# Performance work log

Measured on AMD Instinct MI355X. Metric: run time of the kernel, lower is better.

## Reference

```python
import jax, jax.numpy as jnp
import numpy as np
import math
from jax import lax

TAU = 2
SIGMA_D2 = (TAU / 1.5) ** 2
SIGMA_TH2 = math.radians(20.0) ** 2

_offs = range(-TAU, TAU + 1)
OFFSETS = np.array([(dz, dy, dx) for dz in _offs for dy in _offs for dx in _offs
                    if dz or dy or dx], dtype=np.int32)  # (124, 3)
W_DIST = np.exp(-(OFFSETS.astype(np.float64) ** 2).sum(1) / SIGMA_D2).astype(np.float32)


def setup_inputs() -> dict:
    key = jax.random.key(0)
    k1, k2 = jax.random.split(key)
    n_pred = jax.random.normal(k1, (2, 3, 64, 64, 64), dtype=jnp.float32)
    source_pred = jax.random.normal(k2, (2, 1, 64, 64, 64), dtype=jnp.float32)
    return {"n_pred": n_pred, "source_pred": source_pred}


def reference(n_pred, source_pred):
    B, C, D, H, W = n_pred.shape
    pad = TAU
    # F.normalize(p=2, dim=1, eps=1e-6): divide by max(norm, eps)
    norm = jnp.sqrt(jnp.sum(n_pred * n_pred, axis=1, keepdims=True))
    n = n_pred / jnp.maximum(norm, 1e-6)

    prob = jax.nn.sigmoid(source_pred)            # (B,1,D,H,W)
    central_mask = prob > 0.5                      # (B,1,D,H,W)

    spat = ((0, 0), (0, 0), (pad, pad), (pad, pad), (pad, pad))
    padded_n = jnp.pad(n, spat)                    # zero pad like F.pad value=0
    padded_p = jnp.pad(prob, spat)

    offsets = jnp.asarray(OFFSETS)                 # (124,3)
    w_dist = jnp.asarray(W_DIST, dtype=n.dtype)    # (124,)

    def body(carry, xs):
        off, wd = xs
        start_n = (0, 0, pad + off[0], pad + off[1], pad + off[2])
        shifted_n = lax.dynamic_slice(padded_n, start_n, (B, C, D, H, W))
        shifted_p = lax.dynamic_slice(padded_p, start_n, (B, 1, D, H, W))
        dot = jnp.clip(jnp.sum(n * shifted_n, axis=1), -1.0, 1.0)  # (B,D,H,W)
        theta2 = jnp.arccos(dot) ** 2
        w_theta = jnp.exp(-theta2 / SIGMA_TH2)
        m = (central_mask & (shifted_p > 0.5))[:, 0].astype(n.dtype)  # (B,D,H,W)
        total, count = carry
        total = total + wd * jnp.sum(w_theta * m)
        count = count + jnp.sum(m)
        return (total, count), None

    init = (jnp.zeros((), n.dtype), jnp.zeros((), n.dtype))
    (total, count), _ = lax.scan(body, init, (offsets, w_dist))
    # reduction='mean' over masked elements; 0 if no valid pairs
    return jnp.where(count == 0, jnp.zeros((), n.dtype), total / count)
```

## Files before the change

kernel.cpp:

```cpp
#include <hip/hip_runtime.h>
#include <math.h>

#define PD 68
#define PD2 (PD * PD)
#define PVOL (PD * PD * PD)
#define NBLK2 2048

#define KE (-16.4140429822f)


__global__ __launch_bounds__(256) void pad_normalize_kernel(
    const float* __restrict__ n_pred,
    const float* __restrict__ src,
    float4* __restrict__ q)
{
    int idx = blockIdx.x * 256 + threadIdx.x;
    if (idx >= 2 * PVOL) return;
    int b = idx / PVOL;
    int r = idx - b * PVOL;
    int z = r / PD2;
    int r2 = r - z * PD2;
    int y = r2 / PD;
    int x = r2 - y * PD;
    int gx = x - 2, gy = y - 2, gz = z - 2;
    float4 v = make_float4(0.f, 0.f, 0.f, 0.f);
    if ((unsigned)gx < 64u && (unsigned)gy < 64u && (unsigned)gz < 64u) {
        const size_t cs = 262144;
        size_t vox = ((size_t)gz * 64 + gy) * 64 + gx;
        size_t off = (size_t)b * 3 * cs + vox;
        float xx = n_pred[off];
        float yy = n_pred[off + cs];
        float zz = n_pred[off + 2 * cs];
        float inv = 1.0f / fmaxf(sqrtf(xx * xx + yy * yy + zz * zz), 1e-6f);
        float m = (src[(size_t)b * cs + vox] > 0.0f) ? 1.0f : 0.0f;
        v = make_float4(xx * inv, yy * inv, zz * inv, m);
    }
    q[idx] = v;
}


__global__ __launch_bounds__(256) void stencil_kernel(
    const float4* __restrict__ q, float2* __restrict__ partials)
{
    int x = threadIdx.x & 63;
    int y = blockIdx.x * 4 + (threadIdx.x >> 6);
    int z = blockIdx.y;
    int b = blockIdx.z;
    const float4* cp =
        q + (size_t)b * PVOL + ((size_t)(z + 2) * PD + (y + 2)) * PD + (x + 2);
    float4 c = cp[0];
    float tot = 0.0f, cf = 0.0f;
    if (c.w != 0.0f) {
#pragma unroll
        for (int dz = 0; dz <= 2; ++dz) {
#pragma unroll
            for (int dy = -2; dy <= 2; ++dy) {
#pragma unroll
                for (int dx = -2; dx <= 2; ++dx) {
                    if (dz == 0 && dy < 0) continue;
                    if (dz == 0 && dy == 0 && dx <= 0) continue;
                    const float coff =
                        -0.5625f * (float)(dz * dz + dy * dy + dx * dx);
                    float4 nb = cp[(dz * PD + dy) * PD + dx];
                    float dot = fmaf(c.x, nb.x, fmaf(c.y, nb.y, c.z * nb.z));
                    float u = 1.0f - dot;
                    float p = fmaf(u, 1.8990885e-3f, 5.5803571e-3f);
                    p = fmaf(u, p, 1.8750000e-2f);
                    p = fmaf(u, p, 8.3333333e-2f);
                    p = fmaf(u, p, 1.0f);
                    float uh = u * p * p;
                    float w = __expf(fmaf(KE, uh, coff));
                    tot = fmaf(w, nb.w, tot);
                    cf += nb.w;
                }
            }
        }
    }
#pragma unroll
    for (int s = 32; s > 0; s >>= 1) {
        tot += __shfl_down(tot, s, 64);
        cf  += __shfl_down(cf, s, 64);
    }
    __shared__ float sd[4], sc[4];
    int wid = threadIdx.x >> 6, lane = threadIdx.x & 63;
    if (lane == 0) { sd[wid] = tot; sc[wid] = cf; }
    __syncthreads();
    if (threadIdx.x == 0) {
        int bid = ((int)blockIdx.z * gridDim.y + blockIdx.y) * gridDim.x
                  + blockIdx.x;
        partials[bid] = make_float2(sd[0] + sd[1] + sd[2] + sd[3],
                                    sc[0] + sc[1] + sc[2] + sc[3]);
    }
}

__global__ __launch_bounds__(256) void reduce_kernel(
    const float2* __restrict__ partials, float* __restrict__ out)
{
    double t = 0.0, c = 0.0;
    for (int i = threadIdx.x; i < NBLK2; i += 256) {
        float2 p = partials[i];
        t += (double)p.x;
        c += (double)p.y;
    }
#pragma unroll
    for (int s = 32; s > 0; s >>= 1) {
        t += __shfl_down(t, s, 64);
        c += __shfl_down(c, s, 64);
    }
    __shared__ double sd[4], sc[4];
    int wid = threadIdx.x >> 6, lane = threadIdx.x & 63;
    if (lane == 0) { sd[wid] = t; sc[wid] = c; }
    __syncthreads();
    if (threadIdx.x == 0) {
        double T = sd[0] + sd[1] + sd[2] + sd[3];
        double C = sc[0] + sc[1] + sc[2] + sc[3];
        out[0] = (C == 0.0) ? 0.0f : (float)(T / C);
    }
}


#define TILE 8
#define HALO 2
#define LDIM 12
#define LSZ  1728
#define NVOX 512

__global__ __launch_bounds__(256) void repulsion_fused_kernel(
    const float* __restrict__ n_pred, const float* __restrict__ src,
    double* __restrict__ acc)
{
    __shared__ float4 sn[LSZ];
    __shared__ float rd[4], rc[4];
    const int tx = blockIdx.x * TILE, ty = blockIdx.y * TILE;
    const int b = blockIdx.z >> 3, tz = (blockIdx.z & 7) * TILE;
    const size_t cs = 262144;
    const float* npb = n_pred + (size_t)b * 3 * cs;
    const float* spb = src + (size_t)b * cs;
    for (int i = threadIdx.x; i < LSZ; i += 256) {
        int lx = i % LDIM, t = i / LDIM, ly = t % LDIM, lz = t / LDIM;
        int gx = tx + lx - HALO, gy = ty + ly - HALO, gz = tz + lz - HALO;
        float4 v = make_float4(0.f, 0.f, 0.f, 0.f);
        if ((unsigned)gx < 64u && (unsigned)gy < 64u && (unsigned)gz < 64u) {
            size_t off = ((size_t)gz * 64 + gy) * 64 + gx;
            float xx = npb[off], yy = npb[cs + off], zz = npb[2 * cs + off];
            float inv = 1.0f / fmaxf(sqrtf(xx * xx + yy * yy + zz * zz), 1e-6f);
            float m = (spb[off] > 0.0f) ? 1.0f : 0.0f;
            v = make_float4(xx * inv, yy * inv, zz * inv, m);
        }
        sn[i] = v;
    }
    __syncthreads();
    float tot = 0.0f, cf = 0.0f;
    for (int v = threadIdx.x; v < NVOX; v += 256) {
        int lx = (v & 7) + HALO, ly = ((v >> 3) & 7) + HALO, lz = (v >> 6) + HALO;
        int ci = (lz * LDIM + ly) * LDIM + lx;
        float4 c = sn[ci];
        if (c.w == 0.0f) continue;
#pragma unroll
        for (int dz = -2; dz <= 2; ++dz)
#pragma unroll
            for (int dy = -2; dy <= 2; ++dy)
#pragma unroll
                for (int dx = -2; dx <= 2; ++dx) {
                    if (dz == 0 && dy == 0 && dx == 0) continue;
                    const float coff =
                        -0.5625f * (float)(dz * dz + dy * dy + dx * dx);
                    float4 nb = sn[ci + (dz * LDIM + dy) * LDIM + dx];
                    float dot = fmaf(c.x, nb.x, fmaf(c.y, nb.y, c.z * nb.z));
                    float u = 1.0f - dot;
                    float p = fmaf(u, 1.8990885e-3f, 5.5803571e-3f);
                    p = fmaf(u, p, 1.8750000e-2f);
                    p = fmaf(u, p, 8.3333333e-2f);
                    p = fmaf(u, p, 1.0f);
                    float uh = u * p * p;
                    float w = __expf(fmaf(KE, uh, coff));
                    tot = fmaf(w, nb.w, tot);
                    cf += nb.w;
                }
    }
#pragma unroll
    for (int s = 32; s > 0; s >>= 1) {
        tot += __shfl_down(tot, s, 64);
        cf  += __shfl_down(cf, s, 64);
    }
    int wid = threadIdx.x >> 6, lane = threadIdx.x & 63;
    if (lane == 0) { rd[wid] = tot; rc[wid] = cf; }
    __syncthreads();
    if (threadIdx.x == 0) {
        atomicAdd(&acc[0], (double)rd[0] + rd[1] + rd[2] + rd[3]);
        atomicAdd(&acc[1], (double)rc[0] + rc[1] + rc[2] + rc[3]);
    }
}

__global__ void zero_acc_kernel(double* acc) { acc[0] = 0.0; acc[1] = 0.0; }

__global__ void finalize_kernel(const double* acc, float* out) {
    out[0] = (acc[1] == 0.0) ? 0.0f : (float)(acc[0] / acc[1]);
}


extern "C" void kernel_launch(void* const* d_in, const int* in_sizes, int n_in,
                              void* d_out, int out_size, void* d_ws, size_t ws_size,
                              hipStream_t stream) {
    const float* n_pred = (const float*)d_in[0];
    const float* src    = (const float*)d_in[1];

    const size_t vol_bytes = (size_t)2 * PVOL * sizeof(float4);
    const size_t need = vol_bytes + (size_t)NBLK2 * sizeof(float2);

    if (ws_size >= need) {
        float4* q = (float4*)d_ws;
        float2* partials = (float2*)((char*)d_ws + vol_bytes);
        int nblk = (2 * PVOL + 255) / 256;
        pad_normalize_kernel<<<nblk, 256, 0, stream>>>(n_pred, src, q);
        dim3 grid(16, 64, 2);
        stencil_kernel<<<grid, 256, 0, stream>>>(q, partials);
        reduce_kernel<<<1, 256, 0, stream>>>(partials, (float*)d_out);
    } else {
        double* acc = (double*)d_ws;
        zero_acc_kernel<<<1, 1, 0, stream>>>(acc);
        dim3 grid(8, 8, 16);
        repulsion_fused_kernel<<<grid, 256, 0, stream>>>(n_pred, src, acc);
        finalize_kernel<<<1, 1, 0, stream>>>(acc, (float*)d_out);
    }
}
```

Measured before the change: 32.88 us.

## Process two z-slices per thread to reuse neighbor loads in stencil

```diff
diff --git a/kernel.cpp b/kernel.cpp
--- a/kernel.cpp
+++ b/kernel.cpp
@@ -4,7 +4,7 @@
 #define PD 68
 #define PD2 (PD * PD)
 #define PVOL (PD * PD * PD)
-#define NBLK2 2048
+#define NBLK2 1024
 
 #define KE (-16.4140429822f)
 
@@ -39,43 +39,68 @@
 }
 
 
-__global__ __launch_bounds__(256) void stencil_kernel(
+__global__ __launch_bounds__(256) void stencil_col2_kernel(
     const float4* __restrict__ q, float2* __restrict__ partials)
 {
     int x = threadIdx.x & 63;
     int y = blockIdx.x * 4 + (threadIdx.x >> 6);
-    int z = blockIdx.y;
+    int z0 = blockIdx.y * 2;
     int b = blockIdx.z;
-    const float4* cp =
-        q + (size_t)b * PVOL + ((size_t)(z + 2) * PD + (y + 2)) * PD + (x + 2);
-    float4 c = cp[0];
+    const float4* base =
+        q + (size_t)b * PVOL + ((size_t)(z0 + 2) * PD + (y + 2)) * PD + (x + 2);
+
+    float4 c0 = base[0];
+    float4 c1 = base[PD2];
+
     float tot = 0.0f, cf = 0.0f;
-    if (c.w != 0.0f) {
-#pragma unroll
-        for (int dz = 0; dz <= 2; ++dz) {
-#pragma unroll
-            for (int dy = -2; dy <= 2; ++dy) {
-#pragma unroll
-                for (int dx = -2; dx <= 2; ++dx) {
-                    if (dz == 0 && dy < 0) continue;
-                    if (dz == 0 && dy == 0 && dx <= 0) continue;
-                    const float coff =
-                        -0.5625f * (float)(dz * dz + dy * dy + dx * dx);
-                    float4 nb = cp[(dz * PD + dy) * PD + dx];
-                    float dot = fmaf(c.x, nb.x, fmaf(c.y, nb.y, c.z * nb.z));
-                    float u = 1.0f - dot;
-                    float p = fmaf(u, 1.8990885e-3f, 5.5803571e-3f);
-                    p = fmaf(u, p, 1.8750000e-2f);
-                    p = fmaf(u, p, 8.3333333e-2f);
-                    p = fmaf(u, p, 1.0f);
-                    float uh = u * p * p;
-                    float w = __expf(fmaf(KE, uh, coff));
-                    tot = fmaf(w, nb.w, tot);
-                    cf += nb.w;
+
+    auto app = [&](const float4& c, const float4& nb, float coff) {
+        float dot = fmaf(c.x, nb.x, fmaf(c.y, nb.y, c.z * nb.z));
+        float u = 1.0f - dot;
+        float p = fmaf(u, 1.8990885e-3f, 5.5803571e-3f);
+        p = fmaf(u, p, 1.8750000e-2f);
+        p = fmaf(u, p, 8.3333333e-2f);
+        p = fmaf(u, p, 1.0f);
+        float uh = u * p * p;
+        float w = __expf(fmaf(KE, uh, coff));
+        float g = nb.w * c.w;
+        tot = fmaf(w, g, tot);
+        cf += g;
+    };
+
+    if (c0.w + c1.w != 0.0f) {
+#pragma unroll
+        for (int dy = -2; dy <= 2; ++dy) {
+#pragma unroll
+            for (int dx = -2; dx <= 2; ++dx) {
+                if (dy > 0 || (dy == 0 && dx > 0)) {
+                    float4 nb = base[dy * PD + dx];
+                    app(c0, nb, -0.5625f * (float)(dy * dy + dx * dx));
                 }
             }
         }
-    }
+#pragma unroll
+        for (int k = 1; k <= 3; ++k) {
+#pragma unroll
+            for (int dy = -2; dy <= 2; ++dy) {
+#pragma unroll
+                for (int dx = -2; dx <= 2; ++dx) {
+                    float4 nb = base[k * PD2 + dy * PD + dx];
+                    const int d2 = dy * dy + dx * dx;
+                    if (k <= 2)
+                        app(c0, nb, -0.5625f * (float)(k * k + d2));
+                    const int dz1 = k - 1;
+                    if (dz1 == 0) {
+                        if (dy > 0 || (dy == 0 && dx > 0))
+                            app(c1, nb, -0.5625f * (float)d2);
+                    } else {
+                        app(c1, nb, -0.5625f * (float)(dz1 * dz1 + d2));
+                    }
+                }
+            }
+        }
+    }
+
 #pragma unroll
     for (int s = 32; s > 0; s >>= 1) {
         tot += __shfl_down(tot, s, 64);
@@ -213,8 +238,8 @@
         float2* partials = (float2*)((char*)d_ws + vol_bytes);
         int nblk = (2 * PVOL + 255) / 256;
         pad_normalize_kernel<<<nblk, 256, 0, stream>>>(n_pred, src, q);
-        dim3 grid(16, 64, 2);
-        stencil_kernel<<<grid, 256, 0, stream>>>(q, partials);
+        dim3 grid(16, 32, 2);
+        stencil_col2_kernel<<<grid, 256, 0, stream>>>(q, partials);
         reduce_kernel<<<1, 256, 0, stream>>>(partials, (float*)d_out);
     } else {
         double* acc = (double*)d_ws;
```

Measured after the change: 30.38 us, median of 2. -7.6%, faster.
